# Optimization experiments

Measured on AMD Instinct MI355X. Metric: run time of the kernel, lower is better.

Reference implementation:

```python
import jax, jax.numpy as jnp
import numpy as np

EPS = 1e-8
Q_MAX = 127.0  # 2**(8-1) - 1


def _activation_quant(x):
    gamma = jnp.maximum(jnp.max(jnp.abs(x)), EPS)
    scale = Q_MAX / gamma
    x_int = jnp.clip(jnp.round(x * scale), -Q_MAX, Q_MAX)
    x_fq = x_int / scale
    # straight-through estimator
    return x + jax.lax.stop_gradient(x_fq - x)


def _weight_quant(w):
    gamma = jnp.maximum(jnp.mean(jnp.abs(w)), EPS)
    w_int = jnp.clip(jnp.round(w / gamma), -1.0, 1.0)
    w_fq = w_int * gamma
    return w + jax.lax.stop_gradient(w_fq - w)


def setup_inputs() -> dict:
    key = jax.random.key(0)
    kx, kw, kb = jax.random.split(key, 3)
    in_features, out_features = 2048, 2048
    x = jax.random.normal(kx, (4, 4096, in_features), dtype=jnp.float32)
    # nn.Linear default init: U(-1/sqrt(fan_in), 1/sqrt(fan_in))
    bound = 1.0 / np.sqrt(in_features)
    W = jax.random.uniform(kw, (out_features, in_features), dtype=jnp.float32,
                           minval=-bound, maxval=bound)
    b = jax.random.uniform(kb, (out_features,), dtype=jnp.float32,
                           minval=-bound, maxval=bound)
    return {"x": x, "W": W, "b": b}


def reference(x, W, b):
    x_q = _activation_quant(x)          # int8 absmax fake-quant
    w_q = _weight_quant(W)              # ternary {-g, 0, g} fake-quant
    # F.linear: x @ W^T + b
    return jnp.einsum('bsi,oi->bso', x_q, w_q) + b
```

## Files before the change

kernel.cpp:

```cpp
#include <hip/hip_runtime.h>
#include <hip/hip_bf16.h>
#include <stdint.h>

typedef __attribute__((ext_vector_type(4))) int i32x4;

static constexpr long M_ = 16384;
static constexpr long N_ = 2048;
static constexpr long K_ = 2048;


#define GLOAD_LDS16(g, l)                                                          \
  __builtin_amdgcn_global_load_lds(                                               \
      (const __attribute__((address_space(1))) unsigned int*)(g),                 \
      (__attribute__((address_space(3))) unsigned int*)(l), 16, 0, 0)

__global__ __launch_bounds__(256) void k_stats(const float4* __restrict__ x,
                                               const float4* __restrict__ w,
                                               unsigned* __restrict__ gx_bits,
                                               double* __restrict__ gw_sum) {
  const int b = blockIdx.x;
  const int lane = threadIdx.x & 63, wv = threadIdx.x >> 6;
  if (b < 2048) {
    const long S = 524288;
    long i = (long)b * 256 + threadIdx.x;
    float m0 = 0.f, m1 = 0.f, m2 = 0.f, m3 = 0.f;
#pragma unroll
    for (int it = 0; it < 4; ++it) {
      float4 v0 = x[i];
      float4 v1 = x[i + S];
      float4 v2 = x[i + 2 * S];
      float4 v3 = x[i + 3 * S];
      m0 = fmaxf(m0, fmaxf(fmaxf(fabsf(v0.x), fabsf(v0.y)), fmaxf(fabsf(v0.z), fabsf(v0.w))));
      m1 = fmaxf(m1, fmaxf(fmaxf(fabsf(v1.x), fabsf(v1.y)), fmaxf(fabsf(v1.z), fabsf(v1.w))));
      m2 = fmaxf(m2, fmaxf(fmaxf(fabsf(v2.x), fabsf(v2.y)), fmaxf(fabsf(v2.z), fabsf(v2.w))));
      m3 = fmaxf(m3, fmaxf(fmaxf(fabsf(v3.x), fabsf(v3.y)), fmaxf(fabsf(v3.z), fabsf(v3.w))));
      i += 4 * S;
    }
    float m = fmaxf(fmaxf(m0, m1), fmaxf(m2, m3));
#pragma unroll
    for (int off = 32; off > 0; off >>= 1) m = fmaxf(m, __shfl_down(m, off));
    __shared__ float sm[4];
    if (lane == 0) sm[wv] = m;
    __syncthreads();
    if (threadIdx.x == 0) {
      float bm = fmaxf(fmaxf(sm[0], sm[1]), fmaxf(sm[2], sm[3]));
      atomicMax(gx_bits, __float_as_uint(bm));
    }
  } else {
    const long S = 131072;
    long i = (long)(b - 2048) * 256 + threadIdx.x;
    double s = 0.0;
#pragma unroll
    for (int it = 0; it < 8; ++it) {
      float4 v = w[i];
      s += (double)fabsf(v.x) + (double)fabsf(v.y) + (double)fabsf(v.z) + (double)fabsf(v.w);
      i += S;
    }
#pragma unroll
    for (int off = 32; off > 0; off >>= 1) s += __shfl_down(s, off);
    __shared__ double sd[4];
    if (lane == 0) sd[wv] = s;
    __syncthreads();
    if (threadIdx.x == 0) atomicAdd(gw_sum, (sd[0] + sd[1]) + (sd[2] + sd[3]));
  }
}

__global__ __launch_bounds__(256) void k_quant(const float4* __restrict__ x,
                                               const float4* __restrict__ w,
                                               char4* __restrict__ xq,
                                               char4* __restrict__ wq,
                                               const unsigned* __restrict__ gx_bits,
                                               const double* __restrict__ gw_sum) {
  const int b = blockIdx.x;
  if (b < 2048) {
    const double gx = (double)fmaxf(__uint_as_float(*gx_bits), 1e-8f);
    const double scale = 127.0 / gx;
    const long S = 524288;
    long i = (long)b * 256 + threadIdx.x;
#pragma unroll
    for (int it = 0; it < 16; ++it) {
      float4 v = x[i];
      char4 o;
      o.x = (signed char)(int)fmin(fmax(rint((double)v.x * scale), -127.0), 127.0);
      o.y = (signed char)(int)fmin(fmax(rint((double)v.y * scale), -127.0), 127.0);
      o.z = (signed char)(int)fmin(fmax(rint((double)v.z * scale), -127.0), 127.0);
      o.w = (signed char)(int)fmin(fmax(rint((double)v.w * scale), -127.0), 127.0);
      xq[i] = o;
      i += S;
    }
  } else {
    const double gw = fmax(*gw_sum * (1.0 / 4194304.0), 1e-8);
    const double inv = 1.0 / gw;
    const long S = 131072;
    long i = (long)(b - 2048) * 256 + threadIdx.x;
#pragma unroll
    for (int it = 0; it < 8; ++it) {
      float4 v = w[i];
      char4 o;
      o.x = (signed char)(int)fmin(fmax(rint((double)v.x * inv), -1.0), 1.0);
      o.y = (signed char)(int)fmin(fmax(rint((double)v.y * inv), -1.0), 1.0);
      o.z = (signed char)(int)fmin(fmax(rint((double)v.z * inv), -1.0), 1.0);
      o.w = (signed char)(int)fmin(fmax(rint((double)v.w * inv), -1.0), 1.0);
      wq[i] = o;
      i += S;
    }
  }
}


template <int BUF>
__device__ __forceinline__ void stageA(signed char* lds, const signed char* gp, int kb,
                                       int goA, int wslotA) {
  constexpr int R = BUF * 8192;
  GLOAD_LDS16(gp + kb + goA, lds + R + wslotA);
  GLOAD_LDS16(gp + kb + goA + 16 * 2048, lds + R + wslotA + 1024);
}

template <int BUF>
__device__ __forceinline__ void stageB(signed char* lds, const signed char* gp, int kb,
                                       int goB, int wslotB) {
  constexpr int R = 16384 + BUF * 16384;
  GLOAD_LDS16(gp + kb + goB, lds + R + wslotB);
  GLOAD_LDS16(gp + kb + goB + 16 * 2048, lds + R + wslotB + 1024);
  GLOAD_LDS16(gp + kb + goB + 32 * 2048, lds + R + wslotB + 2048);
  GLOAD_LDS16(gp + kb + goB + 48 * 2048, lds + R + wslotB + 3072);
}

template <int C>
__device__ __forceinline__ void kstep(signed char* lds, const signed char* Ap,
                                      const signed char* Bp, int kb,
                                      const signed char* pA, const signed char* pB,
                                      int goA, int goB, int wslotA, int wslotB,
                                      i32x4 acc[8][4]) {
  constexpr int RA = C * 8192;
  constexpr int RB = 16384 + C * 16384;
  i32x4 b4[4], a4[4];
#pragma unroll
  for (int n = 0; n < 4; ++n) b4[n] = *(const i32x4*)(pB + RB + n * 1024);
#pragma unroll
  for (int m = 0; m < 4; ++m) a4[m] = *(const i32x4*)(pA + RA + m * 1024);
  stageA<C ^ 1>(lds, Ap, kb, goA, wslotA);
  __builtin_amdgcn_s_barrier();
  asm volatile("s_waitcnt lgkmcnt(0)" ::: "memory");
  __builtin_amdgcn_s_setprio(1);
#pragma unroll
  for (int m = 0; m < 4; ++m)
#pragma unroll
    for (int n = 0; n < 4; ++n)
      acc[m][n] = __builtin_amdgcn_mfma_i32_16x16x64_i8(a4[m], b4[n], acc[m][n], 0, 0, 0);
  __builtin_amdgcn_s_setprio(0);
#pragma unroll
  for (int m = 0; m < 4; ++m) a4[m] = *(const i32x4*)(pA + RA + 4096 + m * 1024);
  stageB<C ^ 1>(lds, Bp, kb, goB, wslotB);
  __builtin_amdgcn_s_barrier();
  asm volatile("s_waitcnt lgkmcnt(0)" ::: "memory");
  __builtin_amdgcn_s_setprio(1);
#pragma unroll
  for (int m = 0; m < 4; ++m)
#pragma unroll
    for (int n = 0; n < 4; ++n)
      acc[4 + m][n] =
          __builtin_amdgcn_mfma_i32_16x16x64_i8(a4[m], b4[n], acc[4 + m][n], 0, 0, 0);
  __builtin_amdgcn_s_setprio(0);
  asm volatile("s_waitcnt vmcnt(0)" ::: "memory");
  __builtin_amdgcn_s_barrier();
}

__global__ __launch_bounds__(256, 2) void k_gemm(
    const signed char* __restrict__ Aq, const signed char* __restrict__ Bq,
    const float* __restrict__ bias, float* __restrict__ out,
    const unsigned* __restrict__ gx_bits, const double* __restrict__ gw_sum) {
  extern __shared__ signed char lds[];

  const int tid = threadIdx.x;
  const int lane = tid & 63;
  const int wid = tid >> 6;
  const int l15 = lane & 15;

  const int wg = (int)((blockIdx.x & 7) * 128 + (blockIdx.x >> 3));
  const int nblk = wg & 7;
  const int mblk = wg >> 3;
  const long brow = (long)mblk * 128;
  const long bcol = (long)nblk * 256;

  const signed char* Ap = Aq + brow * K_;
  const signed char* Bp = Bq + bcol * K_;

  const int swz = ((lane >> 4) ^ ((l15 >> 1) & 3)) << 4;
  const signed char* pA = lds + l15 * 64 + swz;
  const signed char* pB = lds + (wid * 64 + l15) * 64 + swz;

  const int c0 = (lane & 3) ^ ((lane >> 3) & 3);
  const int goA = (wid * 32 + (lane >> 2)) * (int)K_ + c0 * 16;
  const int goB = (wid * 64 + (lane >> 2)) * (int)K_ + c0 * 16;
  const int wslotA = wid * 2048;
  const int wslotB = wid * 4096;

  i32x4 acc[8][4];
#pragma unroll
  for (int m = 0; m < 8; m++)
#pragma unroll
    for (int n = 0; n < 4; n++) acc[m][n] = (i32x4){0, 0, 0, 0};

  stageA<0>(lds, Ap, 0, goA, wslotA);
  stageB<0>(lds, Bp, 0, goB, wslotB);
  asm volatile("s_waitcnt vmcnt(0)" ::: "memory");
  __builtin_amdgcn_s_barrier();

  for (int kt = 0; kt < (int)K_; kt += 128) {
    const int kb0 = kt + 64;
    const int kb1 = (kt + 128) & 2047;
    kstep<0>(lds, Ap, Bp, kb0, pA, pB, goA, goB, wslotA, wslotB, acc);
    kstep<1>(lds, Ap, Bp, kb1, pA, pB, goA, goB, wslotA, wslotB, acc);
  }

  const float gxf = fmaxf(__uint_as_float(*gx_bits), 1e-8f);
  const double gwd = fmax(*gw_sum * (1.0 / 4194304.0), 1e-8);
  const float alpha = (float)((double)gxf * gwd * (1.0 / 127.0));

#pragma unroll
  for (int n = 0; n < 4; ++n) {
    const long col = bcol + wid * 64 + n * 16 + l15;
    const float bv = bias[col];
#pragma unroll
    for (int m = 0; m < 8; ++m) {
      const long row0 = brow + m * 16 + (lane >> 4) * 4;
#pragma unroll
      for (int r = 0; r < 4; ++r) {
        out[(row0 + r) * N_ + col] = (float)acc[m][n][r] * alpha + bv;
      }
    }
  }
}

extern "C" void kernel_launch(void* const* d_in, const int* in_sizes, int n_in,
                              void* d_out, int out_size, void* d_ws, size_t ws_size,
                              hipStream_t stream) {
  const float* x = (const float*)d_in[0];
  const float* W = (const float*)d_in[1];
  const float* b = (const float*)d_in[2];
  float* out = (float*)d_out;

  char* ws = (char*)d_ws;
  double* gw_sum = (double*)ws;
  unsigned* gx_bits = (unsigned*)(ws + 8);
  signed char* xq = (signed char*)(ws + 256);
  signed char* wq = (signed char*)(ws + 256 + (size_t)M_ * (size_t)K_);

  hipMemsetAsync(ws, 0, 16, stream);
  hipLaunchKernelGGL(k_stats, dim3(2560), dim3(256), 0, stream,
                     (const float4*)x, (const float4*)W, gx_bits, gw_sum);
  hipLaunchKernelGGL(k_quant, dim3(2560), dim3(256), 0, stream,
                     (const float4*)x, (const float4*)W, (char4*)xq, (char4*)wq,
                     gx_bits, gw_sum);
  hipLaunchKernelGGL(k_gemm, dim3((unsigned)((M_ / 128) * (N_ / 256))), dim3(256),
                     49152, stream, xq, wq, b, out, gx_bits, gw_sum);
}
```

Before: 158.3 us.

## Switch GEMM to 128x128 tiles with 2x2 wave layout and higher occupancy

```diff
diff --git a/kernel.cpp b/kernel.cpp
--- a/kernel.cpp
+++ b/kernel.cpp
@@ -108,40 +108,32 @@
 }
 
 
-template <int BUF>
-__device__ __forceinline__ void stageA(signed char* lds, const signed char* gp, int kb,
-                                       int goA, int wslotA) {
-  constexpr int R = BUF * 8192;
-  GLOAD_LDS16(gp + kb + goA, lds + R + wslotA);
-  GLOAD_LDS16(gp + kb + goA + 16 * 2048, lds + R + wslotA + 1024);
-}
-
-template <int BUF>
-__device__ __forceinline__ void stageB(signed char* lds, const signed char* gp, int kb,
-                                       int goB, int wslotB) {
-  constexpr int R = 16384 + BUF * 16384;
-  GLOAD_LDS16(gp + kb + goB, lds + R + wslotB);
-  GLOAD_LDS16(gp + kb + goB + 16 * 2048, lds + R + wslotB + 1024);
-  GLOAD_LDS16(gp + kb + goB + 32 * 2048, lds + R + wslotB + 2048);
-  GLOAD_LDS16(gp + kb + goB + 48 * 2048, lds + R + wslotB + 3072);
+template <int ISB, int BUF>
+__device__ __forceinline__ void stage(signed char* lds, const signed char* gp, int kb,
+                                      int go0, int wslot) {
+  constexpr int R = ISB * 16384 + BUF * 8192;
+  GLOAD_LDS16(gp + kb + go0, lds + R + wslot);
+  GLOAD_LDS16(gp + kb + go0 + 16 * 2048, lds + R + wslot + 1024);
 }
 
 template <int C>
 __device__ __forceinline__ void kstep(signed char* lds, const signed char* Ap,
                                       const signed char* Bp, int kb,
                                       const signed char* pA, const signed char* pB,
-                                      int goA, int goB, int wslotA, int wslotB,
-                                      i32x4 acc[8][4]) {
+                                      int go0, int wslot, i32x4 acc[4][4]) {
   constexpr int RA = C * 8192;
-  constexpr int RB = 16384 + C * 16384;
-  i32x4 b4[4], a4[4];
+  constexpr int RB = 16384 + C * 8192;
+  i32x4 a4[4], b4[4];
 #pragma unroll
   for (int n = 0; n < 4; ++n) b4[n] = *(const i32x4*)(pB + RB + n * 1024);
 #pragma unroll
   for (int m = 0; m < 4; ++m) a4[m] = *(const i32x4*)(pA + RA + m * 1024);
-  stageA<C ^ 1>(lds, Ap, kb, goA, wslotA);
-  __builtin_amdgcn_s_barrier();
+
+  stage<0, C ^ 1>(lds, Ap, kb, go0, wslot);
+  stage<1, C ^ 1>(lds, Bp, kb, go0, wslot);
+
   asm volatile("s_waitcnt lgkmcnt(0)" ::: "memory");
+  __builtin_amdgcn_sched_barrier(0);
   __builtin_amdgcn_s_setprio(1);
 #pragma unroll
   for (int m = 0; m < 4; ++m)
@@ -149,69 +141,54 @@
     for (int n = 0; n < 4; ++n)
       acc[m][n] = __builtin_amdgcn_mfma_i32_16x16x64_i8(a4[m], b4[n], acc[m][n], 0, 0, 0);
   __builtin_amdgcn_s_setprio(0);
-#pragma unroll
-  for (int m = 0; m < 4; ++m) a4[m] = *(const i32x4*)(pA + RA + 4096 + m * 1024);
-  stageB<C ^ 1>(lds, Bp, kb, goB, wslotB);
-  __builtin_amdgcn_s_barrier();
-  asm volatile("s_waitcnt lgkmcnt(0)" ::: "memory");
-  __builtin_amdgcn_s_setprio(1);
-#pragma unroll
-  for (int m = 0; m < 4; ++m)
-#pragma unroll
-    for (int n = 0; n < 4; ++n)
-      acc[4 + m][n] =
-          __builtin_amdgcn_mfma_i32_16x16x64_i8(a4[m], b4[n], acc[4 + m][n], 0, 0, 0);
-  __builtin_amdgcn_s_setprio(0);
   asm volatile("s_waitcnt vmcnt(0)" ::: "memory");
   __builtin_amdgcn_s_barrier();
 }
 
-__global__ __launch_bounds__(256, 2) void k_gemm(
+__global__ __launch_bounds__(256, 4) void k_gemm(
     const signed char* __restrict__ Aq, const signed char* __restrict__ Bq,
     const float* __restrict__ bias, float* __restrict__ out,
     const unsigned* __restrict__ gx_bits, const double* __restrict__ gw_sum) {
-  extern __shared__ signed char lds[];
+  __shared__ signed char lds[32768];
 
   const int tid = threadIdx.x;
   const int lane = tid & 63;
   const int wid = tid >> 6;
+  const int wave_m = wid >> 1;
+  const int wave_n = wid & 1;
   const int l15 = lane & 15;
 
-  const int wg = (int)((blockIdx.x & 7) * 128 + (blockIdx.x >> 3));
-  const int nblk = wg & 7;
-  const int mblk = wg >> 3;
+  const int wg = (int)((blockIdx.x & 7) * 256 + (blockIdx.x >> 3));
+  const int nblk = wg & 15;
+  const int mblk = wg >> 4;
   const long brow = (long)mblk * 128;
-  const long bcol = (long)nblk * 256;
+  const long bcol = (long)nblk * 128;
 
   const signed char* Ap = Aq + brow * K_;
   const signed char* Bp = Bq + bcol * K_;
 
   const int swz = ((lane >> 4) ^ ((l15 >> 1) & 3)) << 4;
-  const signed char* pA = lds + l15 * 64 + swz;
-  const signed char* pB = lds + (wid * 64 + l15) * 64 + swz;
+  const signed char* pA = lds + (wave_m * 64 + l15) * 64 + swz;
+  const signed char* pB = lds + (wave_n * 64 + l15) * 64 + swz;
 
   const int c0 = (lane & 3) ^ ((lane >> 3) & 3);
-  const int goA = (wid * 32 + (lane >> 2)) * (int)K_ + c0 * 16;
-  const int goB = (wid * 64 + (lane >> 2)) * (int)K_ + c0 * 16;
-  const int wslotA = wid * 2048;
-  const int wslotB = wid * 4096;
-
-  i32x4 acc[8][4];
-#pragma unroll
-  for (int m = 0; m < 8; m++)
+  const int go0 = (wid * 32 + (lane >> 2)) * (int)K_ + c0 * 16;
+  const int wslot = wid * 2048;
+
+  i32x4 acc[4][4];
+#pragma unroll
+  for (int m = 0; m < 4; m++)
 #pragma unroll
     for (int n = 0; n < 4; n++) acc[m][n] = (i32x4){0, 0, 0, 0};
 
-  stageA<0>(lds, Ap, 0, goA, wslotA);
-  stageB<0>(lds, Bp, 0, goB, wslotB);
+  stage<0, 0>(lds, Ap, 0, go0, wslot);
+  stage<1, 0>(lds, Bp, 0, go0, wslot);
   asm volatile("s_waitcnt vmcnt(0)" ::: "memory");
   __builtin_amdgcn_s_barrier();
 
   for (int kt = 0; kt < (int)K_; kt += 128) {
-    const int kb0 = kt + 64;
-    const int kb1 = (kt + 128) & 2047;
-    kstep<0>(lds, Ap, Bp, kb0, pA, pB, goA, goB, wslotA, wslotB, acc);
-    kstep<1>(lds, Ap, Bp, kb1, pA, pB, goA, goB, wslotA, wslotB, acc);
+    kstep<0>(lds, Ap, Bp, kt + 64, pA, pB, go0, wslot, acc);
+    kstep<1>(lds, Ap, Bp, (kt + 128) & 2047, pA, pB, go0, wslot, acc);
   }
 
   const float gxf = fmaxf(__uint_as_float(*gx_bits), 1e-8f);
@@ -220,11 +197,11 @@
 
 #pragma unroll
   for (int n = 0; n < 4; ++n) {
-    const long col = bcol + wid * 64 + n * 16 + l15;
+    const long col = bcol + wave_n * 64 + n * 16 + l15;
     const float bv = bias[col];
 #pragma unroll
-    for (int m = 0; m < 8; ++m) {
-      const long row0 = brow + m * 16 + (lane >> 4) * 4;
+    for (int m = 0; m < 4; ++m) {
+      const long row0 = brow + wave_m * 64 + m * 16 + (lane >> 4) * 4;
 #pragma unroll
       for (int r = 0; r < 4; ++r) {
         out[(row0 + r) * N_ + col] = (float)acc[m][n][r] * alpha + bv;
@@ -253,6 +230,6 @@
   hipLaunchKernelGGL(k_quant, dim3(2560), dim3(256), 0, stream,
                      (const float4*)x, (const float4*)W, (char4*)xq, (char4*)wq,
                      gx_bits, gw_sum);
-  hipLaunchKernelGGL(k_gemm, dim3((unsigned)((M_ / 128) * (N_ / 256))), dim3(256),
-                     49152, stream, xq, wq, b, out, gx_bits, gw_sum);
-}
+  hipLaunchKernelGGL(k_gemm, dim3((unsigned)((M_ / 128) * (N_ / 128))), dim3(256),
+                     0, stream, xq, wq, b, out, gx_bits, gw_sum);
+}
```

Result: no change. 160.0 us (+1.1%).
